# Performance work log

Measured on AMD Instinct MI355X. Metric: run time of the kernel, lower is better.

## Reference

```python
import jax, jax.numpy as jnp
import numpy as np

B, T, C = 4, 2048, 1024
H, Dh = 16, 64
EPS = 1e-5

def _layernorm(x, g, b):
    mu = jnp.mean(x, axis=-1, keepdims=True)
    var = jnp.mean(jnp.square(x - mu), axis=-1, keepdims=True)
    return (x - mu) * jax.lax.rsqrt(var + EPS) * g + b

def setup_inputs() -> dict:
    key = jax.random.key(0)
    ks = jax.random.split(key, 12)
    s = lambda fan_in: 1.0 / np.sqrt(fan_in)
    return {
        "x":  jax.random.normal(ks[0], (B, T, C), dtype=jnp.float32),
        "Wq": jax.random.uniform(ks[1], (C, H * Dh), jnp.float32, -s(C), s(C)),
        "Wk": jax.random.uniform(ks[2], (C, H * Dh), jnp.float32, -s(C), s(C)),
        "Wv": jax.random.uniform(ks[3], (C, H * Dh), jnp.float32, -s(C), s(C)),
        "Wo": jax.random.uniform(ks[4], (H * Dh, C), jnp.float32, -s(H * Dh), s(H * Dh)),
        "bo": jnp.zeros((C,), jnp.float32),
        "W1": jax.random.uniform(ks[5], (C, 4 * C), jnp.float32, -s(C), s(C)),
        "b1": jnp.zeros((4 * C,), jnp.float32),
        "W2": jax.random.uniform(ks[6], (4 * C, C), jnp.float32, -s(4 * C), s(4 * C)),
        "b2": jnp.zeros((C,), jnp.float32),
        "g1": jnp.ones((C,), jnp.float32),
        "be1": jnp.zeros((C,), jnp.float32),
        "g2": jnp.ones((C,), jnp.float32),
        "be2": jnp.zeros((C,), jnp.float32),
    }

def reference(x, Wq, Wk, Wv, Wo, bo, W1, b1, W2, b2, g1, be1, g2, be2):
    # --- pre-LN attention ---
    h = _layernorm(x, g1, be1)                                   # [B,T,C]
    q = (h @ Wq).reshape(B, T, H, Dh)                            # per-head projections fused
    k = (h @ Wk).reshape(B, T, H, Dh)
    v = (h @ Wv).reshape(B, T, H, Dh)
    scores = jnp.einsum('bqhd,bkhd->bhqk', q, k) * (Dh ** -0.5)  # [B,H,T,T]
    causal = jnp.tril(jnp.ones((T, T), dtype=bool))
    scores = jnp.where(causal, scores, -jnp.inf)
    wei = jax.nn.softmax(scores, axis=-1)                        # dropout p=0 (eval)
    attn = jnp.einsum('bhqk,bkhd->bqhd', wei, v).reshape(B, T, H * Dh)
    x = x + attn @ Wo + bo
    # --- pre-LN MLP ---
    h2 = _layernorm(x, g2, be2)
    x = x + jax.nn.relu(h2 @ W1 + b1) @ W2 + b2
    return x
```

## Files before the change

### kernel.cpp

```cpp
#include <hip/hip_runtime.h>
#include <hip/hip_bf16.h>

typedef __hip_bfloat16 bf16;
typedef __attribute__((ext_vector_type(8))) short short8;
typedef __attribute__((ext_vector_type(4))) short s16x4;
typedef __attribute__((ext_vector_type(4))) float f32x4;

__device__ __forceinline__ float s2f(short s) {
    unsigned u = ((unsigned)(unsigned short)s) << 16;
    return __builtin_bit_cast(float, u);
}
__device__ __forceinline__ short f2s(float f) {
    bf16 h = __float2bfloat16(f);
    return __builtin_bit_cast(short, h);
}
__device__ __forceinline__ void gload_lds16(const void* g, void* l) {
    __builtin_amdgcn_global_load_lds(
        (const __attribute__((address_space(1))) unsigned int*)g,
        (__attribute__((address_space(3))) unsigned int*)l, 16, 0, 0);
}

__global__ __launch_bounds__(256) void tconv_kernel(const float* __restrict__ src,
                                                    short* __restrict__ dst,
                                                    int R, int C) {
    __shared__ short tile[64][65];
    const int r0 = blockIdx.y * 64, c0 = blockIdx.x * 64;
    const int t = threadIdx.x;
    const int lr = t >> 2, lc = (t & 3) * 16;
    const float* sp = src + (size_t)(r0 + lr) * C + c0 + lc;
#pragma unroll
    for (int q = 0; q < 4; q++) {
        f32x4 v = *(const f32x4*)(const void*)(sp + q * 4);
#pragma unroll
        for (int j = 0; j < 4; j++) tile[lr][lc + q * 4 + j] = f2s(v[j]);
    }
    __syncthreads();
    short8 o0, o1;
#pragma unroll
    for (int j = 0; j < 8; j++) { o0[j] = tile[lc + j][lr]; o1[j] = tile[lc + 8 + j][lr]; }
    short* dp = dst + (size_t)(c0 + lr) * R + r0 + lc;
    *(short8*)(void*)dp = o0;
    *(short8*)(void*)(dp + 8) = o1;
}

__global__ __launch_bounds__(256) void ln_kernel(const float* __restrict__ x,
                                                 const float* __restrict__ g,
                                                 const float* __restrict__ beta,
                                                 bf16* __restrict__ out) {
    const int t = threadIdx.x;
    const int w = t >> 6, lane = t & 63;
    const int row = blockIdx.x * 4 + w;
    const float* xr = x + (size_t)row * 1024;
    float v[16];
    float s = 0.f, ss = 0.f;
#pragma unroll
    for (int p = 0; p < 4; p++) {
        f32x4 xv = *(const f32x4*)(const void*)(xr + p * 256 + lane * 4);
#pragma unroll
        for (int j = 0; j < 4; j++) {
            v[p * 4 + j] = xv[j];
            s += xv[j];
            ss += xv[j] * xv[j];
        }
    }
#pragma unroll
    for (int off = 32; off >= 1; off >>= 1) {
        s += __shfl_xor(s, off);
        ss += __shfl_xor(ss, off);
    }
    const float mu = s * (1.0f / 1024.0f);
    const float var = ss * (1.0f / 1024.0f) - mu * mu;
    const float rstd = rsqrtf(var + 1e-5f);
    short* orow = (short*)(void*)(out + (size_t)row * 1024);
#pragma unroll
    for (int p = 0; p < 4; p++) {
        const int c = p * 256 + lane * 4;
        f32x4 gv = *(const f32x4*)(const void*)(g + c);
        f32x4 bv = *(const f32x4*)(const void*)(beta + c);
        s16x4 o;
#pragma unroll
        for (int j = 0; j < 4; j++)
            o[j] = f2s((v[p * 4 + j] - mu) * rstd * gv[j] + bv[j]);
        *(s16x4*)(void*)(orow + c) = o;
    }
}

__global__ __launch_bounds__(256) void gemm64(const bf16* __restrict__ A,
                                              const bf16* __restrict__ Bt,
                                              const float* __restrict__ bias,
                                              const float* resid,
                                              void* Cp, int c_f32,
                                              int m_base, int N, int K,
                                              int relu_flag) {
    __shared__ short As[64 * 64];
    __shared__ short Bs[64 * 64];

    const int t = threadIdx.x;
    const int m0 = blockIdx.x * 64;
    const int n0 = blockIdx.y * 64;
    const int w = t >> 6;
    const int lane = t & 63;
    const int wm = (w >> 1) * 32;
    const int wn = (w & 1) * 32;

    const int sr = t >> 2, sk = (t & 3) * 8;
    const bf16* aA = A + (size_t)(m0 + sr) * K + sk;
    const bf16* aB = Bt + (size_t)(n0 + sr) * K + sk;
    short* ldsA0 = &As[w * 512];
    short* ldsA1 = &As[2048 + w * 512];
    short* ldsB0 = &Bs[w * 512];
    short* ldsB1 = &Bs[2048 + w * 512];

    const int l = lane & 15;
    const int lk = (lane >> 4) * 8;

    f32x4 acc[2][2] = {};

    for (int k0 = 0; k0 < K; k0 += 64) {
        __syncthreads();
        gload_lds16(aA + k0, ldsA0);
        gload_lds16(aA + k0 + 32, ldsA1);
        gload_lds16(aB + k0, ldsB0);
        gload_lds16(aB + k0 + 32, ldsB1);
        __syncthreads();
#pragma unroll
        for (int ks = 0; ks < 2; ks++) {
            short8 a0 = *(const short8*)&As[ks * 2048 + (wm + l) * 32 + lk];
            short8 a1 = *(const short8*)&As[ks * 2048 + (wm + 16 + l) * 32 + lk];
            short8 b0 = *(const short8*)&Bs[ks * 2048 + (wn + l) * 32 + lk];
            short8 b1 = *(const short8*)&Bs[ks * 2048 + (wn + 16 + l) * 32 + lk];
            acc[0][0] = __builtin_amdgcn_mfma_f32_16x16x32_bf16(a0, b0, acc[0][0], 0, 0, 0);
            acc[0][1] = __builtin_amdgcn_mfma_f32_16x16x32_bf16(a0, b1, acc[0][1], 0, 0, 0);
            acc[1][0] = __builtin_amdgcn_mfma_f32_16x16x32_bf16(a1, b0, acc[1][0], 0, 0, 0);
            acc[1][1] = __builtin_amdgcn_mfma_f32_16x16x32_bf16(a1, b1, acc[1][1], 0, 0, 0);
        }
    }

    const int lrow4 = (lane >> 4) * 4;
#pragma unroll
    for (int mi = 0; mi < 2; mi++)
#pragma unroll
        for (int r = 0; r < 4; r++) {
            const int grow = m_base + m0 + wm + mi * 16 + lrow4 + r;
#pragma unroll
            for (int ni = 0; ni < 2; ni++) {
                const int gcol = n0 + wn + ni * 16 + l;
                float val = acc[mi][ni][r];
                if (bias) val += bias[gcol];
                if (relu_flag) val = fmaxf(val, 0.f);
                const size_t ci = (size_t)grow * N + gcol;
                if (resid) val += resid[ci];
                if (c_f32) ((float*)Cp)[ci] = val;
                else        ((short*)Cp)[ci] = f2s(val);
            }
        }
}

__global__ __launch_bounds__(256) void attn_kernel(const bf16* __restrict__ qkv,
                                                   bf16* __restrict__ o) {
    __shared__ short KsF[64 * 64];
    __shared__ short Vt[64][72];
    __shared__ short Pl[4][32][72];

    const int bh = blockIdx.x;
    const int b = bh >> 4, h = bh & 15;
    const int qt = 15 - blockIdx.y;
    const int q0 = qt * 128;
    const size_t rbase = (size_t)b * 2048;
    const int hcol = h * 64;

    const int t = threadIdx.x;
    const int w = t >> 6;
    const int lane = t & 63;
    const int l = lane & 15;
    const int g = lane >> 4;
    const int sp = t >> 3;
    const int sb = (t & 7) * 8;

    const int qw0 = q0 + 32 * w;
    short8 qf[2][2];
#pragma unroll
    for (int mi = 0; mi < 2; mi++)
#pragma unroll
        for (int ks = 0; ks < 2; ks++) {
            const short* qp = (const short*)qkv +
                (rbase + qw0 + mi * 16 + l) * 3072 + hcol + ks * 32 + g * 8;
            short8 tv = *(const short8*)(const void*)qp;
            short8 sv;
#pragma unroll
            for (int e = 0; e < 8; e++) sv[e] = f2s(s2f(tv[e]) * 0.125f);
            qf[mi][ks] = sv;
        }

    const int key_a = w * 16 + (lane >> 3);
    const int kd = (lane & 7) ^ ((lane >> 3) & 7);
    const short* kgA = (const short*)qkv + (rbase + key_a) * 3072 + 1024 + hcol + kd * 8;
    const short* kgB = kgA + 8 * 3072;
    short* kdstA = &KsF[w * 1024];
    short* kdstB = &KsF[w * 1024 + 512];

    f32x4 o_acc[2][4] = {};
    f32x4 l_acc[2] = {};
    short8 onesf;
    {
        const short ov = (l == 0) ? (short)0x3F80 : (short)0;
#pragma unroll
        for (int e = 0; e < 8; e++) onesf[e] = ov;
    }
    const f32x4 s_init = {-12.f, -12.f, -12.f, -12.f};

    const int kt_max = (q0 + 127) >> 6;
    for (int kt = 0; kt <= kt_max; kt++) {
        const int k0 = kt * 64;
        const short* vg = (const short*)qkv + (rbase + k0 + 2 * sp) * 3072 + 2048 + hcol + sb;
        short8 vv0 = *(const short8*)(const void*)vg;
        short8 vv1 = *(const short8*)(const void*)(vg + 3072);
        __syncthreads();
        gload_lds16(kgA + (size_t)k0 * 3072, kdstA);
        gload_lds16(kgB + (size_t)k0 * 3072, kdstB);
        {
            const int key = 2 * sp;
            const int cbk = key >> 3;
            const int kin = key & 7;
#pragma unroll
            for (int j = 0; j < 8; j++) {
                const int d = sb + j;
                const int col = ((cbk ^ (d >> 3)) << 3) + kin;
                int pk = (int)(unsigned short)vv0[j] | ((int)(unsigned short)vv1[j] << 16);
                *(int*)(void*)&Vt[d][col] = pk;
            }
        }
        __syncthreads();

        if (k0 <= qw0 + 31) {
            const bool needMask = (k0 + 63 > qw0);
            f32x4 s_acc[2][4];
#pragma unroll
            for (int mi = 0; mi < 2; mi++)
#pragma unroll
                for (int ni = 0; ni < 4; ni++) s_acc[mi][ni] = s_init;
#pragma unroll
            for (int ks = 0; ks < 2; ks++) {
                short8 kf[4];
#pragma unroll
                for (int ni = 0; ni < 4; ni++) {
                    const int key = ni * 16 + l;
                    const int c = key * 8 + ((ks * 4 + g) ^ (key & 7));
                    kf[ni] = *(const short8*)&KsF[c * 8];
                }
#pragma unroll
                for (int mi = 0; mi < 2; mi++)
#pragma unroll
                    for (int ni = 0; ni < 4; ni++)
                        s_acc[mi][ni] = __builtin_amdgcn_mfma_f32_16x16x32_bf16(
                            qf[mi][ks], kf[ni], s_acc[mi][ni], 0, 0, 0);
            }
#pragma unroll
            for (int mi = 0; mi < 2; mi++)
#pragma unroll
                for (int r = 0; r < 4; r++) {
                    const int qg = qw0 + mi * 16 + 4 * g + r;
#pragma unroll
                    for (int ni = 0; ni < 4; ni++) {
                        float s = s_acc[mi][ni][r];
                        if (needMask && (k0 + ni * 16 + l > qg)) s = -1e30f;
                        Pl[w][mi * 16 + 4 * g + r][ni * 16 + l] = f2s(__expf(s));
                    }
                }
#pragma unroll
            for (int ks = 0; ks < 2; ks++) {
                short8 pf[2], vf[4];
#pragma unroll
                for (int mi = 0; mi < 2; mi++)
                    pf[mi] = *(const short8*)&Pl[w][mi * 16 + l][ks * 32 + g * 8];
#pragma unroll
                for (int nd = 0; nd < 4; nd++) {
                    const int d = nd * 16 + l;
                    const int cb = ks * 4 + g;
                    vf[nd] = *(const short8*)&Vt[d][((cb ^ (d >> 3)) << 3)];
                }
#pragma unroll
                for (int mi = 0; mi < 2; mi++) {
                    l_acc[mi] = __builtin_amdgcn_mfma_f32_16x16x32_bf16(
                        pf[mi], onesf, l_acc[mi], 0, 0, 0);
#pragma unroll
                    for (int nd = 0; nd < 4; nd++)
                        o_acc[mi][nd] = __builtin_amdgcn_mfma_f32_16x16x32_bf16(
                            pf[mi], vf[nd], o_acc[mi][nd], 0, 0, 0);
                }
            }
        }
    }

#pragma unroll
    for (int mi = 0; mi < 2; mi++)
#pragma unroll
        for (int r = 0; r < 4; r++) {
            float lsum = __shfl(l_acc[mi][r], lane & 48);
            const float inv = 1.0f / lsum;
            const int qg = qw0 + mi * 16 + 4 * g + r;
            short* op = (short*)(void*)(o + (rbase + qg) * 1024 + hcol);
#pragma unroll
            for (int nd = 0; nd < 4; nd++)
                op[nd * 16 + l] = f2s(o_acc[mi][nd][r] * inv);
        }
}

extern "C" void kernel_launch(void* const* d_in, const int* in_sizes, int n_in,
                              void* d_out, int out_size, void* d_ws, size_t ws_size,
                              hipStream_t stream) {
    const float* x   = (const float*)d_in[0];
    const float* Wq  = (const float*)d_in[1];
    const float* Wk  = (const float*)d_in[2];
    const float* Wv  = (const float*)d_in[3];
    const float* Wo  = (const float*)d_in[4];
    const float* bo  = (const float*)d_in[5];
    const float* W1  = (const float*)d_in[6];
    const float* b1  = (const float*)d_in[7];
    const float* W2  = (const float*)d_in[8];
    const float* b2  = (const float*)d_in[9];
    const float* g1  = (const float*)d_in[10];
    const float* be1 = (const float*)d_in[11];
    const float* g2  = (const float*)d_in[12];
    const float* be2 = (const float*)d_in[13];

    char* ws = (char*)d_ws;
    const size_t MB = (size_t)1024 * 1024;
    bf16*  s0  = (bf16*)(ws);
    bf16*  qkv = (bf16*)(ws + 16 * MB);
    short* WoT = (short*)(ws + 16 * MB);
    short* W1T = (short*)(ws);
    short* W2T = (short*)(ws + 8 * MB);
    bf16*  h2  = (bf16*)(ws + 16 * MB);
    bf16*  m1  = (bf16*)(ws + 32 * MB);
    short* WT  = (short*)d_out;
    float* x1  = (float*)d_out;

    const int M = 8192, C = 1024, F = 4096, MH = 4096;

    tconv_kernel<<<dim3(16, 16), 256, 0, stream>>>(Wq, WT,                   C, C);
    tconv_kernel<<<dim3(16, 16), 256, 0, stream>>>(Wk, WT + 1024 * 1024,     C, C);
    tconv_kernel<<<dim3(16, 16), 256, 0, stream>>>(Wv, WT + 2 * 1024 * 1024, C, C);

    ln_kernel<<<M / 4, 256, 0, stream>>>(x, g1, be1, s0);

    gemm64<<<dim3(M / 64, 3072 / 64), 256, 0, stream>>>(
        s0, (const bf16*)WT, nullptr, nullptr, qkv, 0, 0, 3072, C, 0);

    attn_kernel<<<dim3(64, 16), 256, 0, stream>>>(qkv, s0);

    tconv_kernel<<<dim3(16, 16), 256, 0, stream>>>(Wo, WoT, C, C);
    gemm64<<<dim3(M / 64, C / 64), 256, 0, stream>>>(
        s0, (const bf16*)WoT, bo, x, x1, 1, 0, C, C, 0);

    tconv_kernel<<<dim3(64, 16), 256, 0, stream>>>(W1, W1T, C, F);
    tconv_kernel<<<dim3(16, 64), 256, 0, stream>>>(W2, W2T, F, C);

    ln_kernel<<<M / 4, 256, 0, stream>>>(x1, g2, be2, h2);

    for (int half = 0; half < 2; half++) {
        const bf16* Ah = h2 + (size_t)half * MH * C;
        gemm64<<<dim3(MH / 64, F / 64), 256, 0, stream>>>(
            Ah, (const bf16*)W1T, b1, nullptr, m1, 0, 0, F, C, 1);
        gemm64<<<dim3(MH / 64, C / 64), 256, 0, stream>>>(
            m1, (const bf16*)W2T, b2, x1, d_out, 1, half * MH, C, F, 0);
    }
}
```

Before: 594.3 us.

## Enlarge GEMM tiles to 128x128 with 4x4 MFMA per wave and workgroup swizzle

Replaces the 64x64 GEMM kernel with a 128x128 tile where each wave computes a 64x64 sub-tile via 16 MFMA accumulators, using a K-step of 32. A workgroup index swizzle remaps blocks to improve L2 locality across neighbouring tiles. The larger tile raises arithmetic intensity per LDS/global load but increases register pressure and reduces the number of workgroups, which may lower occupancy on smaller GEMMs like the Wo projection.

```diff
diff --git a/kernel.cpp b/kernel.cpp
--- a/kernel.cpp
+++ b/kernel.cpp
@@ -85,65 +85,74 @@
     }
 }
 
-__global__ __launch_bounds__(256) void gemm64(const bf16* __restrict__ A,
-                                              const bf16* __restrict__ Bt,
-                                              const float* __restrict__ bias,
-                                              const float* resid,
-                                              void* Cp, int c_f32,
-                                              int m_base, int N, int K,
-                                              int relu_flag) {
-    __shared__ short As[64 * 64];
-    __shared__ short Bs[64 * 64];
+__global__ __launch_bounds__(256) void gemm128(const bf16* __restrict__ A,
+                                               const bf16* __restrict__ Bt,
+                                               const float* __restrict__ bias,
+                                               const float* resid,
+                                               void* Cp, int c_f32,
+                                               int m_base, int N, int K,
+                                               int relu_flag) {
+    __shared__ short As[128 * 32];
+    __shared__ short Bs[128 * 32];
 
     const int t = threadIdx.x;
-    const int m0 = blockIdx.x * 64;
-    const int n0 = blockIdx.y * 64;
+    const int nwg = gridDim.x * gridDim.y;
+    const int orig = blockIdx.y * gridDim.x + blockIdx.x;
+    const int swz = (orig & 7) * (nwg >> 3) + (orig >> 3);
+    const int bm = swz % gridDim.x;
+    const int bn = swz / gridDim.x;
+    const int m0 = bm * 128;
+    const int n0 = bn * 128;
+
     const int w = t >> 6;
     const int lane = t & 63;
-    const int wm = (w >> 1) * 32;
-    const int wn = (w & 1) * 32;
-
-    const int sr = t >> 2, sk = (t & 3) * 8;
-    const bf16* aA = A + (size_t)(m0 + sr) * K + sk;
-    const bf16* aB = Bt + (size_t)(n0 + sr) * K + sk;
-    short* ldsA0 = &As[w * 512];
-    short* ldsA1 = &As[2048 + w * 512];
-    short* ldsB0 = &Bs[w * 512];
-    short* ldsB1 = &Bs[2048 + w * 512];
+    const int wm = (w >> 1) * 64;
+    const int wn = (w & 1) * 64;
+
+    const int srow = lane >> 2;
+    const int sk = (lane & 3) * 8;
+    const bf16* aA = A + (size_t)(m0 + w * 32 + srow) * K + sk;
+    const bf16* aB = Bt + (size_t)(n0 + w * 32 + srow) * K + sk;
+    short* dA0 = &As[w * 1024];
+    short* dA1 = &As[w * 1024 + 512];
+    short* dB0 = &Bs[w * 1024];
+    short* dB1 = &Bs[w * 1024 + 512];
+    const size_t rowK16 = (size_t)16 * K;
 
     const int l = lane & 15;
-    const int lk = (lane >> 4) * 8;
-
-    f32x4 acc[2][2] = {};
-
-    for (int k0 = 0; k0 < K; k0 += 64) {
+    const int g = lane >> 4;
+
+    f32x4 acc[4][4] = {};
+
+    for (int k0 = 0; k0 < K; k0 += 32) {
         __syncthreads();
-        gload_lds16(aA + k0, ldsA0);
-        gload_lds16(aA + k0 + 32, ldsA1);
-        gload_lds16(aB + k0, ldsB0);
-        gload_lds16(aB + k0 + 32, ldsB1);
+        gload_lds16(aA + k0, dA0);
+        gload_lds16(aA + rowK16 + k0, dA1);
+        gload_lds16(aB + k0, dB0);
+        gload_lds16(aB + rowK16 + k0, dB1);
         __syncthreads();
-#pragma unroll
-        for (int ks = 0; ks < 2; ks++) {
-            short8 a0 = *(const short8*)&As[ks * 2048 + (wm + l) * 32 + lk];
-            short8 a1 = *(const short8*)&As[ks * 2048 + (wm + 16 + l) * 32 + lk];
-            short8 b0 = *(const short8*)&Bs[ks * 2048 + (wn + l) * 32 + lk];
-            short8 b1 = *(const short8*)&Bs[ks * 2048 + (wn + 16 + l) * 32 + lk];
-            acc[0][0] = __builtin_amdgcn_mfma_f32_16x16x32_bf16(a0, b0, acc[0][0], 0, 0, 0);
-            acc[0][1] = __builtin_amdgcn_mfma_f32_16x16x32_bf16(a0, b1, acc[0][1], 0, 0, 0);
-            acc[1][0] = __builtin_amdgcn_mfma_f32_16x16x32_bf16(a1, b0, acc[1][0], 0, 0, 0);
-            acc[1][1] = __builtin_amdgcn_mfma_f32_16x16x32_bf16(a1, b1, acc[1][1], 0, 0, 0);
-        }
-    }
-
-    const int lrow4 = (lane >> 4) * 4;
-#pragma unroll
-    for (int mi = 0; mi < 2; mi++)
+        short8 af[4], bfr[4];
+#pragma unroll
+        for (int i = 0; i < 4; i++) {
+            af[i]  = *(const short8*)&As[(wm + i * 16 + l) * 32 + g * 8];
+            bfr[i] = *(const short8*)&Bs[(wn + i * 16 + l) * 32 + g * 8];
+        }
+#pragma unroll
+        for (int mi = 0; mi < 4; mi++)
+#pragma unroll
+            for (int ni = 0; ni < 4; ni++)
+                acc[mi][ni] = __builtin_amdgcn_mfma_f32_16x16x32_bf16(
+                    af[mi], bfr[ni], acc[mi][ni], 0, 0, 0);
+    }
+
+    const int r4 = g * 4;
+#pragma unroll
+    for (int mi = 0; mi < 4; mi++)
 #pragma unroll
         for (int r = 0; r < 4; r++) {
-            const int grow = m_base + m0 + wm + mi * 16 + lrow4 + r;
-#pragma unroll
-            for (int ni = 0; ni < 2; ni++) {
+            const int grow = m_base + m0 + wm + mi * 16 + r4 + r;
+#pragma unroll
+            for (int ni = 0; ni < 4; ni++) {
                 const int gcol = n0 + wn + ni * 16 + l;
                 float val = acc[mi][ni][r];
                 if (bias) val += bias[gcol];
@@ -151,7 +160,7 @@
                 const size_t ci = (size_t)grow * N + gcol;
                 if (resid) val += resid[ci];
                 if (c_f32) ((float*)Cp)[ci] = val;
-                else        ((short*)Cp)[ci] = f2s(val);
+                else       ((short*)Cp)[ci] = f2s(val);
             }
         }
 }
@@ -344,13 +353,13 @@
 
     ln_kernel<<<M / 4, 256, 0, stream>>>(x, g1, be1, s0);
 
-    gemm64<<<dim3(M / 64, 3072 / 64), 256, 0, stream>>>(
+    gemm128<<<dim3(M / 128, 3072 / 128), 256, 0, stream>>>(
         s0, (const bf16*)WT, nullptr, nullptr, qkv, 0, 0, 3072, C, 0);
 
     attn_kernel<<<dim3(64, 16), 256, 0, stream>>>(qkv, s0);
 
     tconv_kernel<<<dim3(16, 16), 256, 0, stream>>>(Wo, WoT, C, C);
-    gemm64<<<dim3(M / 64, C / 64), 256, 0, stream>>>(
+    gemm128<<<dim3(M / 128, C / 128), 256, 0, stream>>>(
         s0, (const bf16*)WoT, bo, x, x1, 1, 0, C, C, 0);
 
     tconv_kernel<<<dim3(64, 16), 256, 0, stream>>>(W1, W1T, C, F);
@@ -360,9 +369,9 @@
 
     for (int half = 0; half < 2; half++) {
         const bf16* Ah = h2 + (size_t)half * MH * C;
-        gemm64<<<dim3(MH / 64, F / 64), 256, 0, stream>>>(
+        gemm128<<<dim3(MH / 128, F / 128), 256, 0, stream>>>(
             Ah, (const bf16*)W1T, b1, nullptr, m1, 0, 0, F, C, 1);
-        gemm64<<<dim3(MH / 64, C / 64), 256, 0, stream>>>(
+        gemm128<<<dim3(MH / 128, C / 128), 256, 0, stream>>>(
             m1, (const bf16*)W2T, b2, x1, d_out, 1, half * MH, C, F, 0);
     }
 }
```

Measured after the change: 767.6 us. 29.2% more time.

## Add 256x256 double-buffered MFMA GEMM for QKV and W1 projections

Applied to the files above, without the earlier changes.

Adds a gemm256 kernel with a 256x256 output tile and 512 threads. It double-buffers A and B through 128KB of LDS using direct global-to-LDS loads, XOR-swizzled reads, explicit waitcnt/barrier phasing and setprio around the 16x16x32 bf16 MFMA blocks. It replaces the 64x64 GEMM for the QKV projection and the W1 MLP projection, aiming to raise data reuse per tile and overlap loads with compute. The kernel hardcodes K=1024 and assumes dimensions divisible by 256. Its large LDS footprint limits occupancy to one block per CU.

```diff
diff --git a/kernel.cpp b/kernel.cpp
--- a/kernel.cpp
+++ b/kernel.cpp
@@ -19,6 +19,13 @@
         (const __attribute__((address_space(1))) unsigned int*)g,
         (__attribute__((address_space(3))) unsigned int*)l, 16, 0, 0);
 }
+
+#define PH_VM8  asm volatile("s_waitcnt vmcnt(8)" ::: "memory")
+#define PH_VM4  asm volatile("s_waitcnt vmcnt(4)" ::: "memory")
+#define PH_VM0  asm volatile("s_waitcnt vmcnt(0)" ::: "memory")
+#define PH_BAR  __builtin_amdgcn_s_barrier()
+#define PH_LGKM do { asm volatile("s_waitcnt lgkmcnt(0)" ::: "memory"); \
+                     __builtin_amdgcn_sched_barrier(0); } while (0)
 
 __global__ __launch_bounds__(256) void tconv_kernel(const float* __restrict__ src,
                                                     short* __restrict__ dst,
@@ -154,6 +161,133 @@
                 else        ((short*)Cp)[ci] = f2s(val);
             }
         }
+}
+
+#define MM_BLOCK(ACC)                                                        \
+    do {                                                                     \
+        __builtin_amdgcn_s_setprio(1);                                       \
+        _Pragma("unroll")                                                    \
+        for (int mi_ = 0; mi_ < 4; mi_++)                                    \
+            _Pragma("unroll")                                                \
+            for (int ni_ = 0; ni_ < 4; ni_++)                                \
+                ACC[mi_][ni_] = __builtin_amdgcn_mfma_f32_16x16x32_bf16(     \
+                    af[mi_], bf[ni_], ACC[mi_][ni_], 0, 0, 0);               \
+        __builtin_amdgcn_s_setprio(0);                                       \
+    } while (0)
+
+__global__ __launch_bounds__(512, 2) void gemm256(const bf16* __restrict__ A,
+                                                  const bf16* __restrict__ Bt,
+                                                  const float* __restrict__ bias,
+                                                  bf16* __restrict__ Cp,
+                                                  int N, int relu_flag) {
+    __shared__ char lds[131072];
+    constexpr int NT = 16;
+
+    const int t = threadIdx.x;
+    const int w = t >> 6, lane = t & 63;
+    const int l = lane & 15, g = lane >> 4;
+    const int m0 = blockIdx.x * 256, n0 = blockIdx.y * 256;
+    const int wm = (w >> 2) * 128, wn = (w & 3) * 64;
+    const int qx = (g ^ ((l >> 1) & 3)) * 16;
+    const int qh8 = (((lane & 3) ^ ((lane >> 3) & 3)) * 8);
+    const int srow = w * 32 + (lane >> 2);
+    const short* Asrc = (const short*)A;
+    const short* Bsrc = (const short*)Bt;
+
+    f32x4 accL[4][4] = {};
+    f32x4 accH[4][4] = {};
+    short8 af[4], bf[4];
+
+    auto stage = [&](int th, int j) {
+        const int ks = j >> 1, mat = j & 1;
+        char* slot = lds + ((th & 1) << 16) + (mat << 15) + (ks << 14);
+        const short* mp = mat ? Bsrc : Asrc;
+        const int rowb = (mat ? n0 : m0);
+        const int kc = th * 64 + ks * 32 + qh8;
+        gload_lds16(mp + (size_t)(rowb + srow) * 1024 + kc,      slot + (w * 2) * 1024);
+        gload_lds16(mp + (size_t)(rowb + srow + 16) * 1024 + kc, slot + (w * 2 + 1) * 1024);
+    };
+    auto lda = [&](const char* rb, int mi, int ks) -> short8 {
+        return *(const short8*)(rb + (ks << 14) + (wm + mi * 16 + l) * 64 + qx);
+    };
+    auto ldb = [&](const char* rb, int ni, int ks) -> short8 {
+        return *(const short8*)(rb + 32768 + (ks << 14) + (wn + ni * 16 + l) * 64 + qx);
+    };
+
+    stage(0, 0); stage(0, 1); stage(0, 2); stage(0, 3); stage(1, 0); stage(1, 1);
+
+    for (int it = 0; it < NT - 1; ++it) {
+        const char* rb = lds + ((it & 1) << 16);
+        PH_VM8; PH_BAR;
+#pragma unroll
+        for (int i = 0; i < 4; i++) af[i] = lda(rb, i, 0);
+#pragma unroll
+        for (int i = 0; i < 4; i++) bf[i] = ldb(rb, i, 0);
+        stage(it + 1, 2);
+        PH_LGKM;
+        MM_BLOCK(accL);
+#pragma unroll
+        for (int i = 0; i < 4; i++) af[i] = lda(rb, 4 + i, 0);
+        stage(it + 1, 3);
+        PH_BAR; PH_LGKM;
+        MM_BLOCK(accH);
+        PH_VM8; PH_BAR;
+#pragma unroll
+        for (int i = 0; i < 4; i++) af[i] = lda(rb, i, 1);
+#pragma unroll
+        for (int i = 0; i < 4; i++) bf[i] = ldb(rb, i, 1);
+        if (it + 2 < NT) stage(it + 2, 0);
+        PH_LGKM;
+        MM_BLOCK(accL);
+#pragma unroll
+        for (int i = 0; i < 4; i++) af[i] = lda(rb, 4 + i, 1);
+        if (it + 2 < NT) stage(it + 2, 1);
+        PH_BAR; PH_LGKM;
+        MM_BLOCK(accH);
+    }
+    {
+        const char* rb = lds + (((NT - 1) & 1) << 16);
+        PH_VM4; PH_BAR;
+#pragma unroll
+        for (int i = 0; i < 4; i++) af[i] = lda(rb, i, 0);
+#pragma unroll
+        for (int i = 0; i < 4; i++) bf[i] = ldb(rb, i, 0);
+        PH_LGKM;
+        MM_BLOCK(accL);
+#pragma unroll
+        for (int i = 0; i < 4; i++) af[i] = lda(rb, 4 + i, 0);
+        PH_BAR; PH_LGKM;
+        MM_BLOCK(accH);
+        PH_VM0; PH_BAR;
+#pragma unroll
+        for (int i = 0; i < 4; i++) af[i] = lda(rb, i, 1);
+#pragma unroll
+        for (int i = 0; i < 4; i++) bf[i] = ldb(rb, i, 1);
+        PH_LGKM;
+        MM_BLOCK(accL);
+#pragma unroll
+        for (int i = 0; i < 4; i++) af[i] = lda(rb, 4 + i, 1);
+        PH_BAR; PH_LGKM;
+        MM_BLOCK(accH);
+    }
+
+#pragma unroll
+    for (int half = 0; half < 2; half++)
+#pragma unroll
+        for (int mi = 0; mi < 4; mi++)
+#pragma unroll
+            for (int r = 0; r < 4; r++) {
+                const int grow = m0 + wm + (half * 4 + mi) * 16 + g * 4 + r;
+                short* crow = (short*)(void*)Cp + (size_t)grow * N;
+#pragma unroll
+                for (int ni = 0; ni < 4; ni++) {
+                    const int gcol = n0 + wn + ni * 16 + l;
+                    float val = half ? accH[mi][ni][r] : accL[mi][ni][r];
+                    if (bias) val += bias[gcol];
+                    if (relu_flag) val = fmaxf(val, 0.f);
+                    crow[gcol] = f2s(val);
+                }
+            }
 }
 
 __global__ __launch_bounds__(256) void attn_kernel(const bf16* __restrict__ qkv,
@@ -344,8 +478,8 @@
 
     ln_kernel<<<M / 4, 256, 0, stream>>>(x, g1, be1, s0);
 
-    gemm64<<<dim3(M / 64, 3072 / 64), 256, 0, stream>>>(
-        s0, (const bf16*)WT, nullptr, nullptr, qkv, 0, 0, 3072, C, 0);
+    gemm256<<<dim3(M / 256, 3072 / 256), 512, 0, stream>>>(
+        s0, (const bf16*)WT, nullptr, qkv, 3072, 0);
 
     attn_kernel<<<dim3(64, 16), 256, 0, stream>>>(qkv, s0);
 
@@ -360,8 +494,8 @@
 
     for (int half = 0; half < 2; half++) {
         const bf16* Ah = h2 + (size_t)half * MH * C;
-        gemm64<<<dim3(MH / 64, F / 64), 256, 0, stream>>>(
-            Ah, (const bf16*)W1T, b1, nullptr, m1, 0, 0, F, C, 1);
+        gemm256<<<dim3(MH / 256, F / 256), 512, 0, stream>>>(
+            Ah, (const bf16*)W1T, b1, m1, F, 1);
         gemm64<<<dim3(MH / 64, C / 64), 256, 0, stream>>>(
             m1, (const bf16*)W2T, b2, x1, d_out, 1, half * MH, C, F, 0);
     }
```

After: 544.1 us. 8.5% less time.
